# Kernel tuning notes

Measured on AMD Instinct MI355X. Metric: run time of the kernel, lower is better.

## Reference

```python
import jax, jax.numpy as jnp
import numpy as np


def setup_inputs() -> dict:
    key = jax.random.key(0)
    ks = jax.random.split(key, 12)
    B, N, M, C = 2, 20000, 4096, 6
    S, K, J = 2, 25, 64          # scales, grid cells (2*2+1)^2, neighbors per cell
    Cin = C + 2                   # xy coords concatenated to features
    Cout = 64
    xyz = jax.random.normal(ks[0], (B, N, 3), dtype=jnp.float32)
    feature = jax.random.normal(ks[1], (B, N, C), dtype=jnp.float32)
    new_xyz = jax.random.normal(ks[2], (B, M, 3), dtype=jnp.float32)
    idx = jax.random.randint(ks[3], (S, B, M, K, J), 0, N, dtype=jnp.int32)
    weight = jax.random.uniform(ks[4], (S, B, M, K, J), dtype=jnp.float32)
    conv_w = jax.random.normal(ks[5], (Cout, Cin, K), dtype=jnp.float32) * 0.05
    conv_b = jnp.zeros((Cout,), dtype=jnp.float32)
    mlp_w0 = jax.random.normal(ks[6], (128, S * Cout), dtype=jnp.float32) * 0.05
    mlp_b0 = jnp.zeros((128,), dtype=jnp.float32)
    mlp_w1 = jax.random.normal(ks[7], (256, 128), dtype=jnp.float32) * 0.05
    mlp_b1 = jnp.zeros((256,), dtype=jnp.float32)
    return {"xyz": xyz, "feature": feature, "new_xyz": new_xyz, "idx": idx,
            "weight": weight, "conv_w": conv_w, "conv_b": conv_b,
            "mlp_w0": mlp_w0, "mlp_b0": mlp_b0, "mlp_w1": mlp_w1, "mlp_b1": mlp_b1}


def reference(xyz, feature, new_xyz, idx, weight, conv_w, conv_b,
              mlp_w0, mlp_b0, mlp_w1, mlp_b1):
    # xyz_feature = cat(xy, feature): (B, N, Cin)
    xf = jnp.concatenate([xyz[:, :, :2], feature], axis=-1)
    center2 = new_xyz[:, :, :2]  # (B, M, 2); remaining channels of center are zero

    def per_scale(idx_s, w_s):
        # idx_s, w_s: (B, M, K, J). Gather neighbor features then bilinear-weight.
        gathered = jax.vmap(lambda f, i: f[i])(xf, idx_s)     # (B, M, K, J, Cin)
        nf = jnp.einsum('bmkj,bmkjc->bmkc', w_s, gathered)    # (B, M, K, Cin)
        nf = nf.at[..., :2].add(-center2[:, :, None, :])      # subtract center (xy only)
        # conv2d with kernel (1, K) over the neighbor axis + ReLU
        out = jnp.einsum('bmkc,ock->bom', nf, conv_w) + conv_b[None, :, None]
        return jax.nn.relu(out)                                # (B, Cout, M)

    outs = [per_scale(idx[s], weight[s]) for s in range(idx.shape[0])]
    x = jnp.concatenate(outs, axis=1)                          # (B, S*Cout, M)
    # SharedMLP: 1x1 convs with ReLU (bn=False)
    x = jax.nn.relu(jnp.einsum('bcm,oc->bom', x, mlp_w0) + mlp_b0[None, :, None])
    x = jax.nn.relu(jnp.einsum('bcm,oc->bom', x, mlp_w1) + mlp_b1[None, :, None])
    result_feature = jnp.transpose(x, (0, 2, 1))               # (B, M, 256)
    return new_xyz, result_feature
```

## Files before the change

kernel.cpp:

```cpp
#include <hip/hip_runtime.h>
#include <hip/hip_bf16.h>

#define B 2
#define N 20000
#define M 4096
#define S 2
#define K 25
#define J 64
#define KJ (K*J)
#define TC 32
#define XP 36

typedef unsigned int u32;

__global__ __launch_bounds__(256) void prep_kernel(
    const float* __restrict__ xyz, const float* __restrict__ feature,
    const float* __restrict__ new_xyz, const float* __restrict__ conv_w,
    const float* __restrict__ w0, const float* __restrict__ w1,
    __hip_bfloat16* __restrict__ xfh, float* __restrict__ conv_wT,
    float* __restrict__ w0T, float* __restrict__ w1T,
    float* __restrict__ out_newxyz) {
    const int T1 = B * N * 8;
    const int T2 = 208 * 64;
    const int T3 = B * M * 3;
    const int T4 = 128 * 128;
    const int T5 = 128 * 256;
    int e = blockIdx.x * blockDim.x + threadIdx.x;
    if (e < T1) {
        int r = e >> 3, t = e & 7;
        float v = (t < 2) ? xyz[r * 3 + t] : feature[r * 6 + (t - 2)];
        xfh[e] = __float2bfloat16(v);
    } else if (e < T1 + T2) {
        int e2 = e - T1;
        int i = e2 >> 6, o = e2 & 63;
        conv_wT[e2] = (i < 200) ? conv_w[o * 200 + (i & 7) * 25 + (i >> 3)] : 0.f;
    } else if (e < T1 + T2 + T3) {
        int e3 = e - T1 - T2;
        out_newxyz[e3] = new_xyz[e3];
    } else if (e < T1 + T2 + T3 + T4) {
        int e4 = e - T1 - T2 - T3;
        int c = e4 >> 7, o = e4 & 127;
        w0T[e4] = w0[o * 128 + c];
    } else if (e < T1 + T2 + T3 + T4 + T5) {
        int e5 = e - T1 - T2 - T3 - T4;
        int c = e5 >> 8, o = e5 & 255;
        w1T[e5] = w1[o * 128 + c];
    }
}

__global__ __launch_bounds__(256) void gather_conv_kernel(
    const int* __restrict__ idx, const float* __restrict__ weight,
    const float* __restrict__ new_xyz, const uint4* __restrict__ xfh,
    const float* __restrict__ conv_wT, const float* __restrict__ conv_b,
    float* __restrict__ xmid) {
    __shared__ float snf[208];
    __shared__ float spart[4][64];

    int g = blockIdx.x;
    int m = g & (M - 1);
    int sb = g >> 12;
    int b = sb & (B - 1);
    int s = sb >> 1;
    int tid = threadIdx.x;

    if (tid >= 200 && tid < 208) snf[tid] = 0.f;

    if (tid < 200) {
        const int4*   gi4 = (const int4*)  (idx    + (size_t)g * KJ);
        const float4* gw4 = (const float4*)(weight + (size_t)g * KJ);
        int4   ia = gi4[tid * 2], ib = gi4[tid * 2 + 1];
        float4 wa = gw4[tid * 2], wb = gw4[tid * 2 + 1];

        const uint4* xfb = xfh + (size_t)b * N;
        float acc[8] = {0.f,0.f,0.f,0.f,0.f,0.f,0.f,0.f};
        int   rows[8] = {ia.x, ia.y, ia.z, ia.w, ib.x, ib.y, ib.z, ib.w};
        float wsv[8]  = {wa.x, wa.y, wa.z, wa.w, wb.x, wb.y, wb.z, wb.w};
        #pragma unroll
        for (int j = 0; j < 8; ++j) {
            uint4 r = xfb[rows[j]];
            float w = wsv[j];
            acc[0] = fmaf(w, __uint_as_float(r.x << 16),          acc[0]);
            acc[1] = fmaf(w, __uint_as_float(r.x & 0xffff0000u),  acc[1]);
            acc[2] = fmaf(w, __uint_as_float(r.y << 16),          acc[2]);
            acc[3] = fmaf(w, __uint_as_float(r.y & 0xffff0000u),  acc[3]);
            acc[4] = fmaf(w, __uint_as_float(r.z << 16),          acc[4]);
            acc[5] = fmaf(w, __uint_as_float(r.z & 0xffff0000u),  acc[5]);
            acc[6] = fmaf(w, __uint_as_float(r.w << 16),          acc[6]);
            acc[7] = fmaf(w, __uint_as_float(r.w & 0xffff0000u),  acc[7]);
        }
        #pragma unroll
        for (int d = 1; d < 8; d <<= 1) {
            #pragma unroll
            for (int c = 0; c < 8; ++c) acc[c] += __shfl_xor(acc[c], d, 64);
        }
        if ((tid & 7) == 0) {
            int kk = tid >> 3;
            float cx = new_xyz[(b * M + m) * 3 + 0];
            float cy = new_xyz[(b * M + m) * 3 + 1];
            acc[0] -= cx; acc[1] -= cy;
            float4* s4 = (float4*)&snf[kk * 8];
            s4[0] = make_float4(acc[0], acc[1], acc[2], acc[3]);
            s4[1] = make_float4(acc[4], acc[5], acc[6], acc[7]);
        }
    }
    __syncthreads();

    int o = tid & 63, p = tid >> 6;
    const float4* snf4 = (const float4*)snf;
    float acc2 = 0.f;
    #pragma unroll
    for (int q = 0; q < 13; ++q) {
        float4 v = snf4[p * 13 + q];
        int i = (p * 13 + q) * 4;
        acc2 = fmaf(v.x, conv_wT[(i + 0) * 64 + o], acc2);
        acc2 = fmaf(v.y, conv_wT[(i + 1) * 64 + o], acc2);
        acc2 = fmaf(v.z, conv_wT[(i + 2) * 64 + o], acc2);
        acc2 = fmaf(v.w, conv_wT[(i + 3) * 64 + o], acc2);
    }
    spart[p][o] = acc2;
    __syncthreads();

    if (tid < 64) {
        float v = spart[0][tid] + spart[1][tid] + spart[2][tid] + spart[3][tid] + conv_b[tid];
        v = fmaxf(v, 0.f);
        xmid[((size_t)(b * M + m)) * 128 + s * 64 + tid] = v;
    }
}

__global__ __launch_bounds__(256) void mlp0_kernel(
    float* __restrict__ xmid,
    const float* __restrict__ w0T, const float* __restrict__ b0) {
    __shared__ float ws[128 * 128];
    __shared__ float xs[128 * XP];

    int tid = threadIdx.x;
    int col0 = blockIdx.x * TC;

    {
        const float4* w4 = (const float4*)w0T;
        float4* ws4 = (float4*)ws;
        #pragma unroll
        for (int i = 0; i < 16; ++i) ws4[tid + 256 * i] = w4[tid + 256 * i];
    }
    {
        const float4* xm4 = (const float4*)(xmid + (size_t)col0 * 128);
        #pragma unroll
        for (int r = tid; r < 32 * TC; r += 256) {
            int lc = r >> 5, c4 = r & 31;
            float4 v = xm4[lc * 32 + c4];
            int c = c4 * 4;
            xs[(c + 0) * XP + lc] = v.x;
            xs[(c + 1) * XP + lc] = v.y;
            xs[(c + 2) * XP + lc] = v.z;
            xs[(c + 3) * XP + lc] = v.w;
        }
    }
    __syncthreads();

    int og = tid >> 3, cg = tid & 7;
    int o0 = og * 4, lc0 = cg * 4;
    float acc[4][4];
    #pragma unroll
    for (int i = 0; i < 4; ++i) {
        float bv = b0[o0 + i];
        #pragma unroll
        for (int u = 0; u < 4; ++u) acc[i][u] = bv;
    }
    for (int c = 0; c < 128; ++c) {
        float4 xv = *(const float4*)&xs[c * XP + lc0];
        float4 wv = *(const float4*)&ws[c * 128 + o0];
        acc[0][0] = fmaf(wv.x, xv.x, acc[0][0]);
        acc[0][1] = fmaf(wv.x, xv.y, acc[0][1]);
        acc[0][2] = fmaf(wv.x, xv.z, acc[0][2]);
        acc[0][3] = fmaf(wv.x, xv.w, acc[0][3]);
        acc[1][0] = fmaf(wv.y, xv.x, acc[1][0]);
        acc[1][1] = fmaf(wv.y, xv.y, acc[1][1]);
        acc[1][2] = fmaf(wv.y, xv.z, acc[1][2]);
        acc[1][3] = fmaf(wv.y, xv.w, acc[1][3]);
        acc[2][0] = fmaf(wv.z, xv.x, acc[2][0]);
        acc[2][1] = fmaf(wv.z, xv.y, acc[2][1]);
        acc[2][2] = fmaf(wv.z, xv.z, acc[2][2]);
        acc[2][3] = fmaf(wv.z, xv.w, acc[2][3]);
        acc[3][0] = fmaf(wv.w, xv.x, acc[3][0]);
        acc[3][1] = fmaf(wv.w, xv.y, acc[3][1]);
        acc[3][2] = fmaf(wv.w, xv.z, acc[3][2]);
        acc[3][3] = fmaf(wv.w, xv.w, acc[3][3]);
    }
    #pragma unroll
    for (int u = 0; u < 4; ++u) {
        float4 v = make_float4(fmaxf(acc[0][u], 0.f), fmaxf(acc[1][u], 0.f),
                               fmaxf(acc[2][u], 0.f), fmaxf(acc[3][u], 0.f));
        *(float4*)&xmid[(size_t)(col0 + lc0 + u) * 128 + o0] = v;
    }
}

__global__ __launch_bounds__(256) void mlp1_kernel(
    const float* __restrict__ xmid,
    const float* __restrict__ w1T, const float* __restrict__ b1,
    float* __restrict__ out_rf) {
    __shared__ float ws[128 * 256];
    __shared__ float xs[128 * XP];

    int tid = threadIdx.x;
    int col0 = blockIdx.x * TC;

    {
        const float4* w4 = (const float4*)w1T;
        float4* ws4 = (float4*)ws;
        #pragma unroll
        for (int i = 0; i < 32; ++i) ws4[tid + 256 * i] = w4[tid + 256 * i];
    }
    {
        const float4* xm4 = (const float4*)(xmid + (size_t)col0 * 128);
        #pragma unroll
        for (int r = tid; r < 32 * TC; r += 256) {
            int lc = r >> 5, c4 = r & 31;
            float4 v = xm4[lc * 32 + c4];
            int c = c4 * 4;
            xs[(c + 0) * XP + lc] = v.x;
            xs[(c + 1) * XP + lc] = v.y;
            xs[(c + 2) * XP + lc] = v.z;
            xs[(c + 3) * XP + lc] = v.w;
        }
    }
    __syncthreads();

    int og = tid >> 2, cg = tid & 3;
    int o0 = og * 4, lc0 = cg * 8;
    float acc[4][8];
    #pragma unroll
    for (int i = 0; i < 4; ++i) {
        float bv = b1[o0 + i];
        #pragma unroll
        for (int u = 0; u < 8; ++u) acc[i][u] = bv;
    }
    for (int c = 0; c < 128; ++c) {
        float4 xa = *(const float4*)&xs[c * XP + lc0];
        float4 xb = *(const float4*)&xs[c * XP + lc0 + 4];
        float4 wv = *(const float4*)&ws[c * 256 + o0];
        float xv[8] = {xa.x, xa.y, xa.z, xa.w, xb.x, xb.y, xb.z, xb.w};
        #pragma unroll
        for (int u = 0; u < 8; ++u) {
            acc[0][u] = fmaf(wv.x, xv[u], acc[0][u]);
            acc[1][u] = fmaf(wv.y, xv[u], acc[1][u]);
            acc[2][u] = fmaf(wv.z, xv[u], acc[2][u]);
            acc[3][u] = fmaf(wv.w, xv[u], acc[3][u]);
        }
    }
    #pragma unroll
    for (int u = 0; u < 8; ++u) {
        float4 v = make_float4(fmaxf(acc[0][u], 0.f), fmaxf(acc[1][u], 0.f),
                               fmaxf(acc[2][u], 0.f), fmaxf(acc[3][u], 0.f));
        *(float4*)&out_rf[(size_t)(col0 + lc0 + u) * 256 + o0] = v;
    }
}

extern "C" void kernel_launch(void* const* d_in, const int* in_sizes, int n_in,
                              void* d_out, int out_size, void* d_ws, size_t ws_size,
                              hipStream_t stream) {
    const float* xyz     = (const float*)d_in[0];
    const float* feature = (const float*)d_in[1];
    const float* new_xyz = (const float*)d_in[2];
    const int*   idx     = (const int*)  d_in[3];
    const float* weight  = (const float*)d_in[4];
    const float* conv_w  = (const float*)d_in[5];
    const float* conv_b  = (const float*)d_in[6];
    const float* mlp_w0  = (const float*)d_in[7];
    const float* mlp_b0  = (const float*)d_in[8];
    const float* mlp_w1  = (const float*)d_in[9];
    const float* mlp_b1  = (const float*)d_in[10];

    float* out    = (float*)d_out;
    float* out_rf = out + (size_t)B * M * 3;

    float* wsf = (float*)d_ws;
    __hip_bfloat16* xfh = (__hip_bfloat16*)wsf;
    float* conv_wT = wsf + 160000;
    float* xmid    = conv_wT + 13312;
    float* w0T     = xmid + 1048576;
    float* w1T     = w0T + 16384;

    {
        int total = 320000 + 13312 + 24576 + 16384 + 32768;
        int blocks = (total + 255) / 256;
        prep_kernel<<<blocks, 256, 0, stream>>>(xyz, feature, new_xyz, conv_w,
                                                mlp_w0, mlp_w1,
                                                xfh, conv_wT, w0T, w1T, out);
    }
    {
        int blocks = S * B * M;
        gather_conv_kernel<<<blocks, 256, 0, stream>>>(idx, weight, new_xyz,
                                                       (const uint4*)xfh,
                                                       conv_wT, conv_b, xmid);
    }
    {
        int blocks = (B * M) / TC;
        mlp0_kernel<<<blocks, 256, 0, stream>>>(xmid, w0T, mlp_b0);
    }
    {
        int blocks = (B * M) / TC;
        mlp1_kernel<<<blocks, 256, 0, stream>>>(xmid, w1T, mlp_b1, out_rf);
    }
}
```

Before: 384.6 us.

## Batch gather loads via inline asm, unpad LDS tiles, split mlp1 output halves

The gather kernel now issues its eight row loads as one inline-asm block with the sc0 cache modifier and a single waitcnt, so the loads are kept in flight together. The mlp kernels drop the padded LDS stride (36 to 32), which may introduce bank conflicts on the transposed stores. mlp1 splits the 256 outputs across two blocks, halving its LDS footprint and doubling the grid for occupancy, at the cost of loading each x tile twice. The asm volatile block also limits how the compiler can schedule around these loads.

```diff
diff --git a/kernel.cpp b/kernel.cpp
--- a/kernel.cpp
+++ b/kernel.cpp
@@ -9,9 +9,6 @@
 #define J 64
 #define KJ (K*J)
 #define TC 32
-#define XP 36
-
-typedef unsigned int u32;
 
 __global__ __launch_bounds__(256) void prep_kernel(
     const float* __restrict__ xyz, const float* __restrict__ feature,
@@ -72,12 +69,39 @@
         float4 wa = gw4[tid * 2], wb = gw4[tid * 2 + 1];
 
         const uint4* xfb = xfh + (size_t)b * N;
+        float wsv[8]  = {wa.x, wa.y, wa.z, wa.w, wb.x, wb.y, wb.z, wb.w};
+
+        uint4 r0, r1, r2, r3, r4, r5, r6, r7;
+        {
+            const uint4* a0 = xfb + ia.x;
+            const uint4* a1 = xfb + ia.y;
+            const uint4* a2 = xfb + ia.z;
+            const uint4* a3 = xfb + ia.w;
+            const uint4* a4 = xfb + ib.x;
+            const uint4* a5 = xfb + ib.y;
+            const uint4* a6 = xfb + ib.z;
+            const uint4* a7 = xfb + ib.w;
+            asm volatile(
+                "global_load_dwordx4 %0, %8, off sc0\n\t"
+                "global_load_dwordx4 %1, %9, off sc0\n\t"
+                "global_load_dwordx4 %2, %10, off sc0\n\t"
+                "global_load_dwordx4 %3, %11, off sc0\n\t"
+                "global_load_dwordx4 %4, %12, off sc0\n\t"
+                "global_load_dwordx4 %5, %13, off sc0\n\t"
+                "global_load_dwordx4 %6, %14, off sc0\n\t"
+                "global_load_dwordx4 %7, %15, off sc0\n\t"
+                "s_waitcnt vmcnt(0)"
+                : "=&v"(r0), "=&v"(r1), "=&v"(r2), "=&v"(r3),
+                  "=&v"(r4), "=&v"(r5), "=&v"(r6), "=&v"(r7)
+                : "v"(a0), "v"(a1), "v"(a2), "v"(a3),
+                  "v"(a4), "v"(a5), "v"(a6), "v"(a7));
+        }
+
         float acc[8] = {0.f,0.f,0.f,0.f,0.f,0.f,0.f,0.f};
-        int   rows[8] = {ia.x, ia.y, ia.z, ia.w, ib.x, ib.y, ib.z, ib.w};
-        float wsv[8]  = {wa.x, wa.y, wa.z, wa.w, wb.x, wb.y, wb.z, wb.w};
+        uint4 rr[8] = {r0, r1, r2, r3, r4, r5, r6, r7};
         #pragma unroll
         for (int j = 0; j < 8; ++j) {
-            uint4 r = xfb[rows[j]];
+            uint4 r = rr[j];
             float w = wsv[j];
             acc[0] = fmaf(w, __uint_as_float(r.x << 16),          acc[0]);
             acc[1] = fmaf(w, __uint_as_float(r.x & 0xffff0000u),  acc[1]);
@@ -131,7 +155,7 @@
     float* __restrict__ xmid,
     const float* __restrict__ w0T, const float* __restrict__ b0) {
     __shared__ float ws[128 * 128];
-    __shared__ float xs[128 * XP];
+    __shared__ float xs[128 * 32];
 
     int tid = threadIdx.x;
     int col0 = blockIdx.x * TC;
@@ -145,14 +169,14 @@
     {
         const float4* xm4 = (const float4*)(xmid + (size_t)col0 * 128);
         #pragma unroll
-        for (int r = tid; r < 32 * TC; r += 256) {
+        for (int r = tid; r < 1024; r += 256) {
             int lc = r >> 5, c4 = r & 31;
             float4 v = xm4[lc * 32 + c4];
             int c = c4 * 4;
-            xs[(c + 0) * XP + lc] = v.x;
-            xs[(c + 1) * XP + lc] = v.y;
-            xs[(c + 2) * XP + lc] = v.z;
-            xs[(c + 3) * XP + lc] = v.w;
+            xs[(c + 0) * 32 + lc] = v.x;
+            xs[(c + 1) * 32 + lc] = v.y;
+            xs[(c + 2) * 32 + lc] = v.z;
+            xs[(c + 3) * 32 + lc] = v.w;
         }
     }
     __syncthreads();
@@ -167,7 +191,7 @@
         for (int u = 0; u < 4; ++u) acc[i][u] = bv;
     }
     for (int c = 0; c < 128; ++c) {
-        float4 xv = *(const float4*)&xs[c * XP + lc0];
+        float4 xv = *(const float4*)&xs[c * 32 + lc0];
         float4 wv = *(const float4*)&ws[c * 128 + o0];
         acc[0][0] = fmaf(wv.x, xv.x, acc[0][0]);
         acc[0][1] = fmaf(wv.x, xv.y, acc[0][1]);
@@ -198,60 +222,69 @@
     const float* __restrict__ xmid,
     const float* __restrict__ w1T, const float* __restrict__ b1,
     float* __restrict__ out_rf) {
-    __shared__ float ws[128 * 256];
-    __shared__ float xs[128 * XP];
+    __shared__ float ws[128 * 128];
+    __shared__ float xs[128 * 32];
 
     int tid = threadIdx.x;
-    int col0 = blockIdx.x * TC;
-
-    {
-        const float4* w4 = (const float4*)w1T;
-        float4* ws4 = (float4*)ws;
-        #pragma unroll
-        for (int i = 0; i < 32; ++i) ws4[tid + 256 * i] = w4[tid + 256 * i];
+    int bx = blockIdx.x;
+    int col0 = (bx >> 1) * TC;
+    int oH = (bx & 1) * 128;
+
+    {
+        for (int i = tid; i < 4096; i += 256) {
+            int c = i >> 5, q = i & 31;
+            *(float4*)&ws[c * 128 + q * 4] = *(const float4*)&w1T[c * 256 + oH + q * 4];
+        }
     }
     {
         const float4* xm4 = (const float4*)(xmid + (size_t)col0 * 128);
         #pragma unroll
-        for (int r = tid; r < 32 * TC; r += 256) {
+        for (int r = tid; r < 1024; r += 256) {
             int lc = r >> 5, c4 = r & 31;
             float4 v = xm4[lc * 32 + c4];
             int c = c4 * 4;
-            xs[(c + 0) * XP + lc] = v.x;
-            xs[(c + 1) * XP + lc] = v.y;
-            xs[(c + 2) * XP + lc] = v.z;
-            xs[(c + 3) * XP + lc] = v.w;
+            xs[(c + 0) * 32 + lc] = v.x;
+            xs[(c + 1) * 32 + lc] = v.y;
+            xs[(c + 2) * 32 + lc] = v.z;
+            xs[(c + 3) * 32 + lc] = v.w;
         }
     }
     __syncthreads();
 
-    int og = tid >> 2, cg = tid & 3;
-    int o0 = og * 4, lc0 = cg * 8;
-    float acc[4][8];
+    int og = tid >> 3, cg = tid & 7;
+    int o0 = og * 4, lc0 = cg * 4;
+    float acc[4][4];
     #pragma unroll
     for (int i = 0; i < 4; ++i) {
-        float bv = b1[o0 + i];
-        #pragma unroll
-        for (int u = 0; u < 8; ++u) acc[i][u] = bv;
+        float bv = b1[oH + o0 + i];
+        #pragma unroll
+        for (int u = 0; u < 4; ++u) acc[i][u] = bv;
     }
     for (int c = 0; c < 128; ++c) {
-        float4 xa = *(const float4*)&xs[c * XP + lc0];
-        float4 xb = *(const float4*)&xs[c * XP + lc0 + 4];
-        float4 wv = *(const float4*)&ws[c * 256 + o0];
-        float xv[8] = {xa.x, xa.y, xa.z, xa.w, xb.x, xb.y, xb.z, xb.w};
-        #pragma unroll
-        for (int u = 0; u < 8; ++u) {
-            acc[0][u] = fmaf(wv.x, xv[u], acc[0][u]);
-            acc[1][u] = fmaf(wv.y, xv[u], acc[1][u]);
-            acc[2][u] = fmaf(wv.z, xv[u], acc[2][u]);
-            acc[3][u] = fmaf(wv.w, xv[u], acc[3][u]);
-        }
-    }
-    #pragma unroll
-    for (int u = 0; u < 8; ++u) {
+        float4 xv = *(const float4*)&xs[c * 32 + lc0];
+        float4 wv = *(const float4*)&ws[c * 128 + o0];
+        acc[0][0] = fmaf(wv.x, xv.x, acc[0][0]);
+        acc[0][1] = fmaf(wv.x, xv.y, acc[0][1]);
+        acc[0][2] = fmaf(wv.x, xv.z, acc[0][2]);
+        acc[0][3] = fmaf(wv.x, xv.w, acc[0][3]);
+        acc[1][0] = fmaf(wv.y, xv.x, acc[1][0]);
+        acc[1][1] = fmaf(wv.y, xv.y, acc[1][1]);
+        acc[1][2] = fmaf(wv.y, xv.z, acc[1][2]);
+        acc[1][3] = fmaf(wv.y, xv.w, acc[1][3]);
+        acc[2][0] = fmaf(wv.z, xv.x, acc[2][0]);
+        acc[2][1] = fmaf(wv.z, xv.y, acc[2][1]);
+        acc[2][2] = fmaf(wv.z, xv.z, acc[2][2]);
+        acc[2][3] = fmaf(wv.z, xv.w, acc[2][3]);
+        acc[3][0] = fmaf(wv.w, xv.x, acc[3][0]);
+        acc[3][1] = fmaf(wv.w, xv.y, acc[3][1]);
+        acc[3][2] = fmaf(wv.w, xv.z, acc[3][2]);
+        acc[3][3] = fmaf(wv.w, xv.w, acc[3][3]);
+    }
+    #pragma unroll
+    for (int u = 0; u < 4; ++u) {
         float4 v = make_float4(fmaxf(acc[0][u], 0.f), fmaxf(acc[1][u], 0.f),
                                fmaxf(acc[2][u], 0.f), fmaxf(acc[3][u], 0.f));
-        *(float4*)&out_rf[(size_t)(col0 + lc0 + u) * 256 + o0] = v;
+        *(float4*)&out_rf[(size_t)(col0 + lc0 + u) * 256 + oH + o0] = v;
     }
 }
 
@@ -294,11 +327,9 @@
                                                        conv_wT, conv_b, xmid);
     }
     {
-        int blocks = (B * M) / TC;
-        mlp0_kernel<<<blocks, 256, 0, stream>>>(xmid, w0T, mlp_b0);
-    }
-    {
-        int blocks = (B * M) / TC;
-        mlp1_kernel<<<blocks, 256, 0, stream>>>(xmid, w1T, mlp_b1, out_rf);
-    }
-}
+        mlp0_kernel<<<(B * M) / TC, 256, 0, stream>>>(xmid, w0T, mlp_b0);
+    }
+    {
+        mlp1_kernel<<<2 * (B * M) / TC, 256, 0, stream>>>(xmid, w1T, mlp_b1, out_rf);
+    }
+}
```

Result: faster. 364.1 us (median of 2 runs) (-5.3%).
